# Kernel optimization log

Hardware: AMD Instinct MI355X
Metric: run time of the kernel (lower is better)

Reference implementation:

```python
import jax, jax.numpy as jnp
import numpy as np

GRAPH_SIZE = 1024
D_MODEL = 256
BATCH = 32
INITIAL_ALPHA = 1.0


def setup_inputs() -> dict:
    key = jax.random.key(0)
    ks = jax.random.split(key, 10)
    s = 1.0 / np.sqrt(D_MODEL)  # torch Linear default init scale
    inp = {
        "query": jax.random.normal(ks[0], (BATCH, GRAPH_SIZE, D_MODEL), jnp.float32),
        "key_": jax.random.normal(ks[1], (BATCH, GRAPH_SIZE, D_MODEL), jnp.float32),
        "value": jax.random.normal(ks[2], (BATCH, GRAPH_SIZE, D_MODEL), jnp.float32),
        "dist": jax.random.uniform(ks[3], (BATCH, GRAPH_SIZE, GRAPH_SIZE), jnp.float32),
        "Wq": jax.random.uniform(ks[4], (D_MODEL, D_MODEL), jnp.float32, -s, s),
        "bq": jax.random.uniform(ks[5], (D_MODEL,), jnp.float32, -s, s),
        "Wk": jax.random.uniform(ks[6], (D_MODEL, D_MODEL), jnp.float32, -s, s),
        "bk": jax.random.uniform(ks[7], (D_MODEL,), jnp.float32, -s, s),
        "Wv": jax.random.uniform(ks[8], (D_MODEL, D_MODEL), jnp.float32, -s, s),
        "bv": jax.random.uniform(ks[9], (D_MODEL,), jnp.float32, -s, s),
        # alpha_raw = exp(initial_alpha - 1)
        "alpha_raw": jnp.asarray(np.exp(INITIAL_ALPHA - 1.0), jnp.float32),
    }
    return inp


def reference(query, key_, value, dist, Wq, bq, Wk, bk, Wv, bv, alpha_raw):
    # self-attention path: mask=None, cross=False, query_size == graph_size
    log2_N = jnp.log2(jnp.asarray(GRAPH_SIZE, jnp.float32))
    alpha = jax.nn.softplus(alpha_raw) + 1e-6

    q = jnp.einsum('bnd,ed->bne', query, Wq) + bq   # fc_q
    k = jnp.einsum('bnd,ed->bne', key_, Wk) + bk    # fc_k
    v = jnp.einsum('bnd,ed->bne', value, Wv) + bv   # fc_v

    exp_A = jnp.exp(-alpha * log2_N * dist)         # [b, n, n]
    exp_K = jnp.exp(k)                              # [b, n, d]

    numerator = jnp.einsum('bqk,bkd->bqd', exp_A, exp_K * v)
    denominator = jnp.einsum('bqk,bkd->bqd', exp_A, exp_K) + 1e-8
    return jax.nn.sigmoid(q) * (numerator / denominator)
```

## Files before the change

### kernel.cpp

```cpp
#include <hip/hip_runtime.h>
#include <hip/hip_bf16.h>

#define NBATCH 32
#define NG 1024
#define DM 256

typedef short bf16x8 __attribute__((ext_vector_type(8)));
typedef float f32x4 __attribute__((ext_vector_type(4)));
typedef unsigned short u16x4 __attribute__((ext_vector_type(4)));
typedef unsigned short u16x8 __attribute__((ext_vector_type(8)));

static __device__ __forceinline__ unsigned short f2bf(float f) {
    __hip_bfloat16 h = __float2bfloat16(f);
    return *reinterpret_cast<unsigned short*>(&h);
}

static __device__ __forceinline__ void gload16(const void* g, void* l) {
    __builtin_amdgcn_global_load_lds(
        (const __attribute__((address_space(1))) unsigned int*)g,
        (__attribute__((address_space(3))) unsigned int*)l, 16, 0, 0);
}

static __device__ __forceinline__ void wait_vm8_bar() {
    asm volatile("s_waitcnt vmcnt(8)" ::: "memory");
    asm volatile("s_barrier" ::: "memory");
    __builtin_amdgcn_sched_barrier(0);
}
static __device__ __forceinline__ void wait_vm4_bar() {
    asm volatile("s_waitcnt vmcnt(4)" ::: "memory");
    asm volatile("s_barrier" ::: "memory");
    __builtin_amdgcn_sched_barrier(0);
}
static __device__ __forceinline__ void wait_vm0_bar() {
    asm volatile("s_waitcnt vmcnt(0)" ::: "memory");
    asm volatile("s_barrier" ::: "memory");
    __builtin_amdgcn_sched_barrier(0);
}
static __device__ __forceinline__ void bar_only() {
    asm volatile("s_barrier" ::: "memory");
}

__global__ __launch_bounds__(256) void wpack_kernel(
    const float* __restrict__ Wq, const float* __restrict__ Wk,
    const float* __restrict__ Wv, unsigned short* __restrict__ Wb)
{
    const int i4 = (blockIdx.x * 256 + threadIdx.x) * 4;
    const int t = i4 >> 16;
    const int off = i4 & 65535;
    const float* src = (t == 0) ? Wq : (t == 1) ? Wk : Wv;
    float4 v = *(const float4*)(src + off);
    *(u16x4*)(Wb + i4) = (u16x4){ f2bf(v.x), f2bf(v.y), f2bf(v.z), f2bf(v.w) };
}

__global__ __launch_bounds__(256) void conv3_kernel(
    const float* __restrict__ q, const float* __restrict__ k,
    const float* __restrict__ v, unsigned short* __restrict__ Xb)
{
    const int sel = blockIdx.x >> 12;
    const float* src = (sel == 0) ? q : (sel == 1) ? k : v;
    const size_t i8 = (((size_t)(blockIdx.x & 4095)) * 256 + threadIdx.x) * 8;
    float4 a = *(const float4*)(src + i8);
    float4 b = *(const float4*)(src + i8 + 4);
    *(u16x8*)(Xb + (size_t)sel * NBATCH * NG * DM + i8) =
        (u16x8){ f2bf(a.x), f2bf(a.y), f2bf(a.z), f2bf(a.w),
                 f2bf(b.x), f2bf(b.y), f2bf(b.z), f2bf(b.w) };
}

__global__ __launch_bounds__(256) void exp_kernel(
    const float* __restrict__ dist, unsigned short* __restrict__ ea,
    const float* __restrict__ alpha_raw)
{
    const float alpha = log1pf(__expf(alpha_raw[0])) + 1e-6f;
    const float sc = -alpha * 10.0f * 1.44269504088896f;
    const size_t i8 = ((size_t)blockIdx.x * 256 + threadIdx.x) * 8;
    float4 v0 = *(const float4*)(dist + i8);
    float4 v1 = *(const float4*)(dist + i8 + 4);
    u16x8 o = { f2bf(exp2f(sc * v0.x)), f2bf(exp2f(sc * v0.y)),
                f2bf(exp2f(sc * v0.z)), f2bf(exp2f(sc * v0.w)),
                f2bf(exp2f(sc * v1.x)), f2bf(exp2f(sc * v1.y)),
                f2bf(exp2f(sc * v1.z)), f2bf(exp2f(sc * v1.w)) };
    *(u16x8*)(ea + i8) = o;
}

__global__ __launch_bounds__(256) void projq_kernel(
    const unsigned short* __restrict__ Xq,
    const unsigned short* __restrict__ Wb,
    const float* __restrict__ bq,
    float* __restrict__ sigq)
{
    __shared__ __align__(128) unsigned short lds[2][2][128 * 64];

    const int bid = blockIdx.x;
    const int mt = bid >> 1, nt = bid & 1;
    const int tid = threadIdx.x;
    const int w = tid >> 6, lane = tid & 63;
    const int wm = w >> 1, wn = w & 1;
    const int l15 = lane & 15, lhi = lane >> 4;
    const int lr = lane >> 3, sl = lane & 7;
    const int sp = sl ^ lr;

    const char* Abase = (const char*)(Xq + (size_t)mt * 128 * 256);
    const char* Wbase = (const char*)(Wb + (size_t)nt * 128 * 256);

    f32x4 acc[4][4];
    #pragma unroll
    for (int mi = 0; mi < 4; ++mi)
        #pragma unroll
        for (int ni = 0; ni < 4; ++ni)
            acc[mi][ni] = (f32x4){0.f, 0.f, 0.f, 0.f};

    auto STAGE = [&](int buf, int t) {
        #pragma unroll
        for (int i = 0; i < 4; ++i) {
            const int r = w * 32 + i * 8 + lr;
            gload16(Abase + (size_t)r * 512 + t * 128 + sp * 16,
                    (char*)&lds[buf][0][0] + w * 4096 + i * 1024);
            gload16(Wbase + (size_t)r * 512 + t * 128 + sp * 16,
                    (char*)&lds[buf][1][0] + w * 4096 + i * 1024);
        }
    };

    STAGE(0, 0);
    int cur = 0;
    for (int t = 0; t < 4; ++t) {
        if (t < 3) { STAGE(cur ^ 1, t + 1); wait_vm8_bar(); }
        else       { wait_vm0_bar(); }
        const char* Ab = (const char*)&lds[cur][0][0];
        const char* Bb = (const char*)&lds[cur][1][0];
        #pragma unroll
        for (int kk = 0; kk < 2; ++kk) {
            bf16x8 af[4], bfr[4];
            #pragma unroll
            for (int mi = 0; mi < 4; ++mi) {
                const int tr = wm * 64 + mi * 16 + l15;
                af[mi] = *(const bf16x8*)(Ab + ((tr * 128 + kk * 64 + lhi * 16) ^ ((tr & 7) << 4)));
            }
            #pragma unroll
            for (int ni = 0; ni < 4; ++ni) {
                const int tr = wn * 64 + ni * 16 + l15;
                bfr[ni] = *(const bf16x8*)(Bb + ((tr * 128 + kk * 64 + lhi * 16) ^ ((tr & 7) << 4)));
            }
            #pragma unroll
            for (int mi = 0; mi < 4; ++mi)
                #pragma unroll
                for (int ni = 0; ni < 4; ++ni)
                    acc[mi][ni] = __builtin_amdgcn_mfma_f32_16x16x32_bf16(
                        af[mi], bfr[ni], acc[mi][ni], 0, 0, 0);
        }
        bar_only();
        cur ^= 1;
    }

    #pragma unroll
    for (int ni = 0; ni < 4; ++ni) {
        const int c = nt * 128 + wn * 64 + ni * 16 + l15;
        const float bqs = bq[c];
        #pragma unroll
        for (int mi = 0; mi < 4; ++mi)
            #pragma unroll
            for (int r = 0; r < 4; ++r) {
                const size_t R = (size_t)mt * 128 + wm * 64 + mi * 16 + lhi * 4 + r;
                const float qv = acc[mi][ni][r] + bqs;
                sigq[R * DM + c] = 1.0f / (1.0f + __expf(-qv));
            }
    }
}

__global__ __launch_bounds__(256) void projkv_kernel(
    const unsigned short* __restrict__ Xk,
    const unsigned short* __restrict__ Xv,
    const unsigned short* __restrict__ Wkb,
    const unsigned short* __restrict__ Wvb,
    const float* __restrict__ bk, const float* __restrict__ bv,
    unsigned short* __restrict__ Pt)
{
    __shared__ __align__(128) unsigned short lds[2][2][128 * 64];

    const int bid = blockIdx.x;
    const int mt = bid >> 1, nt = bid & 1;
    const int tid = threadIdx.x;
    const int w = tid >> 6, lane = tid & 63;
    const int wm = w >> 1, wn = w & 1;
    const int l15 = lane & 15, lhi = lane >> 4;
    const int lr = lane >> 3, sl = lane & 7;
    const int sp = sl ^ lr;
    const int g16 = (sp & 3) * 16;

    f32x4 kacc[4][4], vacc[4][4];
    #pragma unroll
    for (int mi = 0; mi < 4; ++mi)
        #pragma unroll
        for (int ni = 0; ni < 4; ++ni) {
            kacc[mi][ni] = (f32x4){0.f, 0.f, 0.f, 0.f};
            vacc[mi][ni] = (f32x4){0.f, 0.f, 0.f, 0.f};
        }

    auto STAGE = [&](int buf, int t) {
        #pragma unroll
        for (int i = 0; i < 4; ++i) {
            const int r = w * 32 + i * 8 + lr;
            const char* asrc = (sp < 4 ? (const char*)Xk : (const char*)Xv)
                               + (size_t)(mt * 128 + r) * 512 + t * 64 + g16;
            gload16(asrc, (char*)&lds[buf][0][0] + w * 4096 + i * 1024);
            const char* wsrc = (sp < 4 ? (const char*)Wkb : (const char*)Wvb)
                               + (size_t)(nt * 128 + r) * 512 + t * 64 + g16;
            gload16(wsrc, (char*)&lds[buf][1][0] + w * 4096 + i * 1024);
        }
    };

    STAGE(0, 0);
    int cur = 0;
    for (int t = 0; t < 8; ++t) {
        if (t < 7) { STAGE(cur ^ 1, t + 1); wait_vm8_bar(); }
        else       { wait_vm0_bar(); }
        const char* Ab = (const char*)&lds[cur][0][0];
        const char* Bb = (const char*)&lds[cur][1][0];
        bf16x8 kaf[4], vaf[4], kbf[4], vbf[4];
        #pragma unroll
        for (int mi = 0; mi < 4; ++mi) {
            const int tr = wm * 64 + mi * 16 + l15;
            const int sw = (tr & 7) << 4;
            kaf[mi] = *(const bf16x8*)(Ab + ((tr * 128 + lhi * 16) ^ sw));
            vaf[mi] = *(const bf16x8*)(Ab + ((tr * 128 + 64 + lhi * 16) ^ sw));
        }
        #pragma unroll
        for (int ni = 0; ni < 4; ++ni) {
            const int tr = wn * 64 + ni * 16 + l15;
            const int sw = (tr & 7) << 4;
            kbf[ni] = *(const bf16x8*)(Bb + ((tr * 128 + lhi * 16) ^ sw));
            vbf[ni] = *(const bf16x8*)(Bb + ((tr * 128 + 64 + lhi * 16) ^ sw));
        }
        #pragma unroll
        for (int mi = 0; mi < 4; ++mi)
            #pragma unroll
            for (int ni = 0; ni < 4; ++ni) {
                kacc[mi][ni] = __builtin_amdgcn_mfma_f32_16x16x32_bf16(
                    kaf[mi], kbf[ni], kacc[mi][ni], 0, 0, 0);
                vacc[mi][ni] = __builtin_amdgcn_mfma_f32_16x16x32_bf16(
                    vaf[mi], vbf[ni], vacc[mi][ni], 0, 0, 0);
            }
        bar_only();
        cur ^= 1;
    }

    const int b = (mt * 128) >> 10;
    const int kb0 = (mt * 128) & 1023;
    #pragma unroll
    for (int ni = 0; ni < 4; ++ni) {
        const int c = nt * 128 + wn * 64 + ni * 16 + l15;
        const float bks = bk[c], bvs = bv[c];
        #pragma unroll
        for (int mi = 0; mi < 4; ++mi) {
            unsigned short p1[4], p2[4];
            #pragma unroll
            for (int r = 0; r < 4; ++r) {
                const float ek = __expf(kacc[mi][ni][r] + bks);
                const float vv = vacc[mi][ni][r] + bvs;
                p1[r] = f2bf(ek * vv);
                p2[r] = f2bf(ek);
            }
            const int kidx = kb0 + wm * 64 + mi * 16 + lhi * 4;
            *(u16x4*)&Pt[((size_t)b * 512 + 2 * c    ) * NG + kidx] =
                (u16x4){p1[0], p1[1], p1[2], p1[3]};
            *(u16x4*)&Pt[((size_t)b * 512 + 2 * c + 1) * NG + kidx] =
                (u16x4){p2[0], p2[1], p2[2], p2[3]};
        }
    }
}

__global__ __launch_bounds__(512, 2) void attn_kernel(
    const unsigned short* __restrict__ ea,
    const unsigned short* __restrict__ Pt,
    float* __restrict__ out)
{
    __shared__ __align__(128) char lds[3][2][16384];

    const int bid = blockIdx.x;
    const int l = (bid & 7) * 32 + (bid >> 3);
    const int b = l >> 3;
    const int m = (l >> 1) & 3;
    const int n = l & 1;

    const int tid = threadIdx.x;
    const int w = tid >> 6, lane = tid & 63;
    const int wm = w >> 2, wn = w & 3;
    const int l15 = lane & 15, lhi = lane >> 4;
    const int xv = (l15 >> 1) & 3;

    const int isB = w >> 2;
    const int sw = w & 3;
    const int srow = lane >> 2;
    const int sg = (lane & 3) ^ ((lane >> 3) & 3);

    const char* Abase = (const char*)(ea + ((size_t)b * NG + m * 256) * NG);
    const char* Bbase = (const char*)(Pt + ((size_t)b * 512 + n * 256) * NG);
    const char* Sbase = isB ? Bbase : Abase;

    f32x4 acc[8][4];
    #pragma unroll
    for (int mi = 0; mi < 8; ++mi)
        #pragma unroll
        for (int ni = 0; ni < 4; ++ni)
            acc[mi][ni] = (f32x4){0.f, 0.f, 0.f, 0.f};

    auto STAGE = [&](int slot, int t) {
        #pragma unroll
        for (int i = 0; i < 4; ++i) {
            const int r = sw * 64 + i * 16 + srow;
            gload16(Sbase + (size_t)r * 2048 + t * 64 + sg * 16,
                    &lds[slot][isB][0] + sw * 4096 + i * 1024);
        }
    };

    STAGE(0, 0);
    int s = 0, snext = 1;
    for (int t = 0; t < 32; ++t) {
        if (t < 31) { STAGE(snext, t + 1); wait_vm4_bar(); }
        else        { wait_vm0_bar(); }
        const char* Ab = &lds[s][0][0];
        const char* Bb = &lds[s][1][0];
        __builtin_amdgcn_s_setprio(1);
        bf16x8 af[8], bfr[4];
        #pragma unroll
        for (int mi = 0; mi < 8; ++mi) {
            const int tr = wm * 128 + mi * 16 + l15;
            af[mi] = *(const bf16x8*)(Ab + tr * 64 + ((lhi ^ xv) * 16));
        }
        #pragma unroll
        for (int ni = 0; ni < 4; ++ni) {
            const int tr = wn * 64 + ni * 16 + l15;
            bfr[ni] = *(const bf16x8*)(Bb + tr * 64 + ((lhi ^ xv) * 16));
        }
        #pragma unroll
        for (int mi = 0; mi < 8; ++mi)
            #pragma unroll
            for (int ni = 0; ni < 4; ++ni)
                acc[mi][ni] = __builtin_amdgcn_mfma_f32_16x16x32_bf16(
                    af[mi], bfr[ni], acc[mi][ni], 0, 0, 0);
        __builtin_amdgcn_s_setprio(0);
        s = snext;
        snext = (snext == 2) ? 0 : snext + 1;
    }

    const int parity = lane & 1;
    #pragma unroll
    for (int mi = 0; mi < 8; ++mi)
        #pragma unroll
        for (int ni = 0; ni < 4; ++ni)
            #pragma unroll
            for (int r = 0; r < 4; ++r) {
                const float own = acc[mi][ni][r];
                const float other = __shfl_xor(own, 1, 64);
                if (!parity) {
                    const int colg = n * 256 + wn * 64 + ni * 16 + l15;
                    const int d = colg >> 1;
                    const int rowg = m * 256 + wm * 128 + mi * 16 + lhi * 4 + r;
                    const size_t idx = ((size_t)b * NG + rowg) * DM + d;
                    out[idx] = out[idx] * (own / (other + 1e-8f));
                }
            }
}

extern "C" void kernel_launch(void* const* d_in, const int* in_sizes, int n_in,
                              void* d_out, int out_size, void* d_ws, size_t ws_size,
                              hipStream_t stream) {
    const float* query = (const float*)d_in[0];
    const float* key_  = (const float*)d_in[1];
    const float* value = (const float*)d_in[2];
    const float* dist  = (const float*)d_in[3];
    const float* Wq = (const float*)d_in[4];
    const float* bq = (const float*)d_in[5];
    const float* Wk = (const float*)d_in[6];
    const float* bk = (const float*)d_in[7];
    const float* Wv = (const float*)d_in[8];
    const float* bv = (const float*)d_in[9];
    const float* alpha_raw = (const float*)d_in[10];
    float* out = (float*)d_out;

    unsigned short* Pt = (unsigned short*)d_ws;
    unsigned short* ea = Pt + (size_t)NBATCH * 512 * NG;
    unsigned short* Xb = ea + (size_t)NBATCH * NG * NG;
    const size_t XN = (size_t)NBATCH * NG * DM;
    unsigned short* Wb = Xb + 3 * XN;

    wpack_kernel<<<dim3(192), dim3(256), 0, stream>>>(Wq, Wk, Wv, Wb);
    conv3_kernel<<<dim3(12288), dim3(256), 0, stream>>>(query, key_, value, Xb);

    projq_kernel<<<dim3(512), dim3(256), 0, stream>>>(Xb, Wb, bq, out);
    projkv_kernel<<<dim3(512), dim3(256), 0, stream>>>(
        Xb + XN, Xb + 2 * XN, Wb + 65536, Wb + 131072, bk, bv, Pt);

    exp_kernel<<<dim3(16384), dim3(256), 0, stream>>>(dist, ea, alpha_raw);
    attn_kernel<<<dim3(256), dim3(512), 0, stream>>>(ea, Pt, out);
}
```

Baseline: 181.1 us.

## Store q as bf16, apply sigmoid in attention epilogue, deepen LDS pipeline

The q projection now writes raw q + bias as bf16 to a separate workspace buffer instead of writing fp32 sigmoid(q) into the output. The attention epilogue reads that bf16 q, computes the sigmoid and writes the output once, with no read-modify-write of the fp32 output. This cuts global memory traffic, at the cost of rounding q to bf16 before the sigmoid. The attention kernel's LDS ring also grows from 3 to 4 stages, prefetching two tiles ahead. That raises per-block LDS to 128KB, which likely allows only one block per CU.

Result: slower. 187.5 us (+3.5%).

```diff
diff --git a/kernel.cpp b/kernel.cpp
--- a/kernel.cpp
+++ b/kernel.cpp
@@ -13,6 +13,10 @@
 static __device__ __forceinline__ unsigned short f2bf(float f) {
     __hip_bfloat16 h = __float2bfloat16(f);
     return *reinterpret_cast<unsigned short*>(&h);
+}
+static __device__ __forceinline__ float bf2f(unsigned short u) {
+    unsigned int x = ((unsigned int)u) << 16;
+    return *reinterpret_cast<float*>(&x);
 }
 
 static __device__ __forceinline__ void gload16(const void* g, void* l) {
@@ -86,7 +90,7 @@
     const unsigned short* __restrict__ Xq,
     const unsigned short* __restrict__ Wb,
     const float* __restrict__ bq,
-    float* __restrict__ sigq)
+    unsigned short* __restrict__ qb)
 {
     __shared__ __align__(128) unsigned short lds[2][2][128 * 64];
 
@@ -160,8 +164,7 @@
             #pragma unroll
             for (int r = 0; r < 4; ++r) {
                 const size_t R = (size_t)mt * 128 + wm * 64 + mi * 16 + lhi * 4 + r;
-                const float qv = acc[mi][ni][r] + bqs;
-                sigq[R * DM + c] = 1.0f / (1.0f + __expf(-qv));
+                qb[R * DM + c] = f2bf(acc[mi][ni][r] + bqs);
             }
     }
 }
@@ -271,9 +274,10 @@
 __global__ __launch_bounds__(512, 2) void attn_kernel(
     const unsigned short* __restrict__ ea,
     const unsigned short* __restrict__ Pt,
+    const unsigned short* __restrict__ qb,
     float* __restrict__ out)
 {
-    __shared__ __align__(128) char lds[3][2][16384];
+    __shared__ __align__(128) char lds[4][2][16384];
 
     const int bid = blockIdx.x;
     const int l = (bid & 7) * 32 + (bid >> 3);
@@ -313,12 +317,13 @@
     };
 
     STAGE(0, 0);
-    int s = 0, snext = 1;
+    STAGE(1, 1);
     for (int t = 0; t < 32; ++t) {
-        if (t < 31) { STAGE(snext, t + 1); wait_vm4_bar(); }
-        else        { wait_vm0_bar(); }
-        const char* Ab = &lds[s][0][0];
-        const char* Bb = &lds[s][1][0];
+        if (t < 30)      { STAGE((t + 2) & 3, t + 2); wait_vm8_bar(); }
+        else if (t == 30){ wait_vm4_bar(); }
+        else             { wait_vm0_bar(); }
+        const char* Ab = &lds[t & 3][0][0];
+        const char* Bb = &lds[t & 3][1][0];
         __builtin_amdgcn_s_setprio(1);
         bf16x8 af[8], bfr[4];
         #pragma unroll
@@ -338,8 +343,6 @@
                 acc[mi][ni] = __builtin_amdgcn_mfma_f32_16x16x32_bf16(
                     af[mi], bfr[ni], acc[mi][ni], 0, 0, 0);
         __builtin_amdgcn_s_setprio(0);
-        s = snext;
-        snext = (snext == 2) ? 0 : snext + 1;
     }
 
     const int parity = lane & 1;
@@ -356,7 +359,9 @@
                     const int d = colg >> 1;
                     const int rowg = m * 256 + wm * 128 + mi * 16 + lhi * 4 + r;
                     const size_t idx = ((size_t)b * NG + rowg) * DM + d;
-                    out[idx] = out[idx] * (own / (other + 1e-8f));
+                    const float q = bf2f(qb[idx]);
+                    const float sig = 1.0f / (1.0f + __expf(-q));
+                    out[idx] = sig * (own / (other + 1e-8f));
                 }
             }
 }
@@ -381,15 +386,16 @@
     unsigned short* ea = Pt + (size_t)NBATCH * 512 * NG;
     unsigned short* Xb = ea + (size_t)NBATCH * NG * NG;
     const size_t XN = (size_t)NBATCH * NG * DM;
-    unsigned short* Wb = Xb + 3 * XN;
+    unsigned short* qb = Xb + 3 * XN;
+    unsigned short* Wb = qb + XN;
 
     wpack_kernel<<<dim3(192), dim3(256), 0, stream>>>(Wq, Wk, Wv, Wb);
     conv3_kernel<<<dim3(12288), dim3(256), 0, stream>>>(query, key_, value, Xb);
 
-    projq_kernel<<<dim3(512), dim3(256), 0, stream>>>(Xb, Wb, bq, out);
+    projq_kernel<<<dim3(512), dim3(256), 0, stream>>>(Xb, Wb, bq, qb);
     projkv_kernel<<<dim3(512), dim3(256), 0, stream>>>(
         Xb + XN, Xb + 2 * XN, Wb + 65536, Wb + 131072, bk, bv, Pt);
 
     exp_kernel<<<dim3(16384), dim3(256), 0, stream>>>(dist, ea, alpha_raw);
-    attn_kernel<<<dim3(256), dim3(512), 0, stream>>>(ea, Pt, out);
-}
+    attn_kernel<<<dim3(256), dim3(512), 0, stream>>>(ea, Pt, qb, out);
+}
```
